# Performance work log

Hardware: AMD Instinct MI355X
Metric: run time of the kernel (lower is better)

## Reference

```python
import jax, jax.numpy as jnp
import numpy as np

N_NODES = 100000
N_EDGES = 1600000
IN_DIM = 128
HID = 32
HEADS = 4
OUT_DIM = 40
NEG_SLOPE = 0.2
BN_EPS = 1e-5


def setup_inputs() -> dict:
    key = jax.random.key(0)
    ks = jax.random.split(key, 13)
    x = jax.random.normal(ks[0], (N_NODES, IN_DIM), jnp.float32)
    edge_index = jax.random.randint(ks[1], (2, N_EDGES), 0, N_NODES, dtype=jnp.int32)
    s0 = 1.0 / np.sqrt(IN_DIM)
    s1 = 1.0 / np.sqrt(HEADS * HID)
    return {
        "x": x,
        "edge_index": edge_index,
        # layer 0: GATConv(IN_DIM -> HID, HEADS heads, concat)
        "W0": jax.random.normal(ks[2], (IN_DIM, HEADS * HID), jnp.float32) * s0,
        "a_src0": jax.random.normal(ks[3], (HEADS, HID), jnp.float32) * s0,
        "a_dst0": jax.random.normal(ks[4], (HEADS, HID), jnp.float32) * s0,
        "b0": jnp.zeros((HEADS * HID,), jnp.float32),
        # BatchNorm1d(HEADS*HID)
        "gamma0": jnp.ones((HEADS * HID,), jnp.float32),
        "beta0": jnp.zeros((HEADS * HID,), jnp.float32),
        # layer 1: GATConv(HEADS*HID -> OUT_DIM, 1 head, mean)
        "W1": jax.random.normal(ks[5], (HEADS * HID, OUT_DIM), jnp.float32) * s1,
        "a_src1": jax.random.normal(ks[6], (1, OUT_DIM), jnp.float32) * s1,
        "a_dst1": jax.random.normal(ks[7], (1, OUT_DIM), jnp.float32) * s1,
        "b1": jnp.zeros((OUT_DIM,), jnp.float32),
    }


def gat_conv(x, src, dst, n_nodes, W, a_src, a_dst, b, heads, concat):
    # linear transform: [N, H, C]
    h = (x @ W).reshape(n_nodes, heads, -1)
    # per-node attention logits [N, H]
    alpha_src = (h * a_src).sum(-1)
    alpha_dst = (h * a_dst).sum(-1)
    # per-edge raw attention [E, H]
    e = jax.nn.leaky_relu(alpha_src[src] + alpha_dst[dst], NEG_SLOPE)
    # softmax over incoming edges of each destination node
    m = jax.ops.segment_max(e, dst, num_segments=n_nodes)  # self-loops -> no empty segment
    ex = jnp.exp(e - m[dst])
    den = jax.ops.segment_sum(ex, dst, num_segments=n_nodes)
    # weighted scatter-aggregate of messages [E, H, C] -> [N, H, C]
    out = jax.ops.segment_sum(ex[:, :, None] * h[src], dst, num_segments=n_nodes)
    out = out / den[:, :, None]
    out = out.reshape(n_nodes, -1) if concat else out.mean(axis=1)
    return out + b


def batch_norm(x, gamma, beta):
    mu = x.mean(axis=0)
    var = x.var(axis=0)
    return (x - mu) * jax.lax.rsqrt(var + BN_EPS) * gamma + beta


def reference(x, edge_index, W0, a_src0, a_dst0, b0, gamma0, beta0,
              W1, a_src1, a_dst1, b1):
    n = x.shape[0]
    loop = jnp.arange(n, dtype=edge_index.dtype)
    src = jnp.concatenate([edge_index[0], loop])  # add self-loops (PyG default)
    dst = jnp.concatenate([edge_index[1], loop])
    # layer 0: GATConv -> BN -> ELU (dropout p=0 / eval -> identity)
    h = gat_conv(x, src, dst, n, W0, a_src0, a_dst0, b0, HEADS, True)
    h = jax.nn.elu(batch_norm(h, gamma0, beta0))
    # layer 1: GATConv, 1 head, mean aggregation, no BN/act
    out = gat_conv(h, src, dst, n, W1, a_src1, a_dst1, b1, 1, False)
    return out
```

## Files before the change

kernel.cpp:

```cpp
#include <hip/hip_runtime.h>
#include <hip/hip_bf16.h>
#include <math.h>

#define NN   100000
#define EE   1600000
#define ETOT (NN + EE)
#define IND  128
#define HD   128
#define OD   40
#define NEG  0.2f
#define BNEPS 1e-5f
#define NBKT 16

typedef __attribute__((ext_vector_type(8))) short bf16x8;
typedef __attribute__((ext_vector_type(4))) float f32x4;

__device__ __forceinline__ float lrelu(float x) { return x > 0.f ? x : NEG * x; }

__device__ __forceinline__ unsigned pack_bf16(float a, float b) {
  unsigned ua = __float_as_uint(a), ub = __float_as_uint(b);
  ua = (ua + 0x7fffu + ((ua >> 16) & 1u)) >> 16;
  ub = (ub + 0x7fffu + ((ub >> 16) & 1u)) >> 16;
  return ua | (ub << 16);
}
__device__ __forceinline__ float bf16_lo(unsigned v) { return __uint_as_float(v << 16); }
__device__ __forceinline__ float bf16_hi(unsigned v) { return __uint_as_float(v & 0xffff0000u); }

__global__ void prep_kernel(const float* __restrict__ W0, unsigned* __restrict__ w0t,
                            const int* __restrict__ ei, int* __restrict__ deg,
                            int* __restrict__ rank) {
  int gid = blockIdx.x * blockDim.x + threadIdx.x;
  if (gid < 128 * 64) {
    int n = gid & 127, kp = gid >> 7;
    float lo = W0[(size_t)(2 * kp) * 128 + n];
    float hi = W0[(size_t)(2 * kp + 1) * 128 + n];
    w0t[n * 64 + kp] = pack_bf16(lo, hi);
  }
  int i4 = gid * 4;
  if (i4 >= ETOT) return;
  int4 d;
  if (i4 < EE) d = *(const int4*)&ei[EE + i4];
  else         d = make_int4(i4 - EE, i4 - EE + 1, i4 - EE + 2, i4 - EE + 3);
  int4 r;
  r.x = atomicAdd(&deg[d.x], 1);
  r.y = atomicAdd(&deg[d.y], 1);
  r.z = atomicAdd(&deg[d.z], 1);
  r.w = atomicAdd(&deg[d.w], 1);
  *(int4*)&rank[i4] = r;
}

__global__ __launch_bounds__(256) void gemm0_kernel(const float* __restrict__ x,
                                                    const unsigned* __restrict__ w0t,
                                                    const float* __restrict__ a_src0,
                                                    const float* __restrict__ a_dst0,
                                                    unsigned* __restrict__ h0b,
                                                    float* __restrict__ asrc0,
                                                    float* __restrict__ adst0) {
  __shared__ __align__(16) unsigned As[64][68];
  __shared__ __align__(16) unsigned Wt[128][68];
  int t = threadIdx.x;
  int rowbase = blockIdx.x * 64;
  for (int idx = t; idx < 128 * 64; idx += 256) {
    Wt[idx >> 6][idx & 63] = w0t[idx];
  }
  for (int idx = t; idx < 64 * 64; idx += 256) {
    int row = idx >> 6, kp = idx & 63;
    int r = rowbase + row;
    int rc = r < NN ? r : NN - 1;
    float2 v = *(const float2*)&x[(size_t)rc * 128 + kp * 2];
    As[row][kp] = pack_bf16(v.x, v.y);
  }
  __syncthreads();

  int lane = t & 63, w = t >> 6;
  int mrow = lane & 15, g = lane >> 4;
  f32x4 acc[8];
#pragma unroll
  for (int nt = 0; nt < 8; nt++) acc[nt] = (f32x4){0.f, 0.f, 0.f, 0.f};
#pragma unroll
  for (int ks = 0; ks < 4; ks++) {
    bf16x8 a = *(const bf16x8*)&As[w * 16 + mrow][ks * 16 + g * 4];
#pragma unroll
    for (int nt = 0; nt < 8; nt++) {
      bf16x8 b = *(const bf16x8*)&Wt[nt * 16 + mrow][ks * 16 + g * 4];
      acc[nt] = __builtin_amdgcn_mfma_f32_16x16x32_bf16(a, b, acc[nt], 0, 0, 0);
    }
  }
  int col = lane & 15;
  float as_[8], ad_[8];
#pragma unroll
  for (int nt = 0; nt < 8; nt++) {
    as_[nt] = a_src0[nt * 16 + col];
    ad_[nt] = a_dst0[nt * 16 + col];
  }
#pragma unroll
  for (int reg = 0; reg < 4; reg++) {
    int r = rowbase + w * 16 + g * 4 + reg;
    bool rok = r < NN;
    float hs0 = acc[0][reg] * as_[0] + acc[1][reg] * as_[1];
    float hs1 = acc[2][reg] * as_[2] + acc[3][reg] * as_[3];
    float hs2 = acc[4][reg] * as_[4] + acc[5][reg] * as_[5];
    float hs3 = acc[6][reg] * as_[6] + acc[7][reg] * as_[7];
    float hd0 = acc[0][reg] * ad_[0] + acc[1][reg] * ad_[1];
    float hd1 = acc[2][reg] * ad_[2] + acc[3][reg] * ad_[3];
    float hd2 = acc[4][reg] * ad_[4] + acc[5][reg] * ad_[5];
    float hd3 = acc[6][reg] * ad_[6] + acc[7][reg] * ad_[7];
#pragma unroll
    for (int mk = 1; mk < 16; mk <<= 1) {
      hs0 += __shfl_xor(hs0, mk); hs1 += __shfl_xor(hs1, mk);
      hs2 += __shfl_xor(hs2, mk); hs3 += __shfl_xor(hs3, mk);
      hd0 += __shfl_xor(hd0, mk); hd1 += __shfl_xor(hd1, mk);
      hd2 += __shfl_xor(hd2, mk); hd3 += __shfl_xor(hd3, mk);
    }
    if ((lane & 15) == 0 && rok) {
      asrc0[r * 4 + 0] = hs0; asrc0[r * 4 + 1] = hs1;
      asrc0[r * 4 + 2] = hs2; asrc0[r * 4 + 3] = hs3;
      adst0[r * 4 + 0] = hd0; adst0[r * 4 + 1] = hd1;
      adst0[r * 4 + 2] = hd2; adst0[r * 4 + 3] = hd3;
    }
#pragma unroll
    for (int nt = 0; nt < 8; nt++) {
      float v = acc[nt][reg];
      float nv = __shfl_xor(v, 1);
      if (!(col & 1) && rok) h0b[(size_t)r * 64 + nt * 8 + (col >> 1)] = pack_bf16(v, nv);
    }
  }
}

__global__ __launch_bounds__(256) void scanA_kernel(const int* __restrict__ deg,
                                                    int* __restrict__ scanned,
                                                    int* __restrict__ blocksums) {
  __shared__ int s[256];
  int t = threadIdx.x;
  int i = blockIdx.x * 256 + t;
  int v = (i < NN) ? deg[i] : 0;
  s[t] = v;
  __syncthreads();
  for (int off = 1; off < 256; off <<= 1) {
    int add = (t >= off) ? s[t - off] : 0;
    __syncthreads();
    s[t] += add;
    __syncthreads();
  }
  if (i < NN) scanned[i] = s[t];
  if (t == 255) blocksums[blockIdx.x] = s[255];
}

__global__ __launch_bounds__(512) void scanB_kernel(int* __restrict__ blocksums, int NB) {
  __shared__ int s[512];
  int t = threadIdx.x;
  int v = (t < NB) ? blocksums[t] : 0;
  s[t] = v;
  __syncthreads();
  for (int off = 1; off < 512; off <<= 1) {
    int add = (t >= off) ? s[t - off] : 0;
    __syncthreads();
    s[t] += add;
    __syncthreads();
  }
  if (t < NB) blocksums[t] = s[t] - v;
}

__global__ __launch_bounds__(256) void scanC_kernel(const int* __restrict__ scanned,
                                                    const int* __restrict__ deg,
                                                    const int* __restrict__ blocksums,
                                                    int* __restrict__ rowptr) {
  int i = blockIdx.x * 256 + threadIdx.x;
  if (i < NN) rowptr[i] = blocksums[blockIdx.x] + scanned[i] - deg[i];
  if (i == 0) rowptr[NN] = ETOT;
}

__global__ void scatter_kernel(const int* __restrict__ ei, const int* __restrict__ rowptr,
                               const int* __restrict__ rank, int* __restrict__ csr_src) {
  int i4 = (blockIdx.x * blockDim.x + threadIdx.x) * 4;
  if (i4 >= ETOT) return;
  int4 s, d;
  if (i4 < EE) {
    s = *(const int4*)&ei[i4];
    d = *(const int4*)&ei[EE + i4];
  } else {
    s = make_int4(i4 - EE, i4 - EE + 1, i4 - EE + 2, i4 - EE + 3);
    d = s;
  }
  int4 rk = *(const int4*)&rank[i4];
  int p0 = rowptr[d.x] + rk.x;
  int p1 = rowptr[d.y] + rk.y;
  int p2 = rowptr[d.z] + rk.z;
  int p3 = rowptr[d.w] + rk.w;
  csr_src[p0] = s.x;
  csr_src[p1] = s.y;
  csr_src[p2] = s.z;
  csr_src[p3] = s.w;
}

__global__ __launch_bounds__(256) void agg0_kernel(const int* __restrict__ csr_src,
                                                   const int* __restrict__ rowptr,
                                                   const float* __restrict__ asrc0,
                                                   const float* __restrict__ adst0,
                                                   const unsigned* __restrict__ h0b,
                                                   const float* __restrict__ b0,
                                                   unsigned* __restrict__ agg0b,
                                                   float* __restrict__ bnsumB,
                                                   float* __restrict__ bnsqB) {
  __shared__ float ws[16][4][17];
  __shared__ int   ss[16][16];
  __shared__ float Lsum[4][16][8], Lsq[4][16][8];
  int t = threadIdx.x;
  int grp = t >> 4;
  int p   = t & 15;
  int n = blockIdx.x * 16 + grp;
  int start = rowptr[n], end = rowptr[n + 1];
  float4 ad = *(const float4*)&adst0[(size_t)n * 4];
  int head = p >> 2;
  float a0 = 0.f, a1 = 0.f, a2 = 0.f, a3 = 0.f, a4 = 0.f, a5 = 0.f, a6 = 0.f, a7 = 0.f;
  float d0 = 0.f, d1 = 0.f, d2 = 0.f, d3 = 0.f;

  for (int base = start; base < end; base += 16) {
    int cnt = min(16, end - base);
    if (p < cnt) {
      int s = csr_src[base + p];
      float4 as = *(const float4*)&asrc0[(size_t)s * 4];
      float w0 = __expf(lrelu(as.x + ad.x));
      float w1 = __expf(lrelu(as.y + ad.y));
      float w2 = __expf(lrelu(as.z + ad.z));
      float w3 = __expf(lrelu(as.w + ad.w));
      d0 += w0; d1 += w1; d2 += w2; d3 += w3;
      ss[grp][p] = s;
      ws[grp][0][p] = w0;
      ws[grp][1][p] = w1;
      ws[grp][2][p] = w2;
      ws[grp][3][p] = w3;
    }
    __builtin_amdgcn_wave_barrier();
    for (int eb = 0; eb < cnt; eb += 4) {
      int e0 = eb, e1 = eb + 1, e2 = eb + 2, e3 = eb + 3;
      float w0 = ws[grp][head][e0];
      float w1 = (e1 < cnt) ? ws[grp][head][e1] : 0.f;
      float w2 = (e2 < cnt) ? ws[grp][head][e2] : 0.f;
      float w3 = (e3 < cnt) ? ws[grp][head][e3] : 0.f;
      int s0 = ss[grp][e0];
      int s1 = ss[grp][(e1 < cnt) ? e1 : e0];
      int s2 = ss[grp][(e2 < cnt) ? e2 : e0];
      int s3 = ss[grp][(e3 < cnt) ? e3 : e0];
      uint4 h0v = *(const uint4*)&h0b[(size_t)s0 * 64 + p * 4];
      uint4 h1v = *(const uint4*)&h0b[(size_t)s1 * 64 + p * 4];
      uint4 h2v = *(const uint4*)&h0b[(size_t)s2 * 64 + p * 4];
      uint4 h3v = *(const uint4*)&h0b[(size_t)s3 * 64 + p * 4];
      a0 += w0 * bf16_lo(h0v.x); a1 += w0 * bf16_hi(h0v.x);
      a2 += w0 * bf16_lo(h0v.y); a3 += w0 * bf16_hi(h0v.y);
      a4 += w0 * bf16_lo(h0v.z); a5 += w0 * bf16_hi(h0v.z);
      a6 += w0 * bf16_lo(h0v.w); a7 += w0 * bf16_hi(h0v.w);
      a0 += w1 * bf16_lo(h1v.x); a1 += w1 * bf16_hi(h1v.x);
      a2 += w1 * bf16_lo(h1v.y); a3 += w1 * bf16_hi(h1v.y);
      a4 += w1 * bf16_lo(h1v.z); a5 += w1 * bf16_hi(h1v.z);
      a6 += w1 * bf16_lo(h1v.w); a7 += w1 * bf16_hi(h1v.w);
      a0 += w2 * bf16_lo(h2v.x); a1 += w2 * bf16_hi(h2v.x);
      a2 += w2 * bf16_lo(h2v.y); a3 += w2 * bf16_hi(h2v.y);
      a4 += w2 * bf16_lo(h2v.z); a5 += w2 * bf16_hi(h2v.z);
      a6 += w2 * bf16_lo(h2v.w); a7 += w2 * bf16_hi(h2v.w);
      a0 += w3 * bf16_lo(h3v.x); a1 += w3 * bf16_hi(h3v.x);
      a2 += w3 * bf16_lo(h3v.y); a3 += w3 * bf16_hi(h3v.y);
      a4 += w3 * bf16_lo(h3v.z); a5 += w3 * bf16_hi(h3v.z);
      a6 += w3 * bf16_lo(h3v.w); a7 += w3 * bf16_hi(h3v.w);
    }
    __builtin_amdgcn_wave_barrier();
  }
#pragma unroll
  for (int mk = 1; mk < 16; mk <<= 1) {
    d0 += __shfl_xor(d0, mk);
    d1 += __shfl_xor(d1, mk);
    d2 += __shfl_xor(d2, mk);
    d3 += __shfl_xor(d3, mk);
  }
  float dh = head == 0 ? d0 : head == 1 ? d1 : head == 2 ? d2 : d3;
  float rd = 1.f / dh;
  int c = p * 8;
  float4 b1v = *(const float4*)&b0[c];
  float4 b2v = *(const float4*)&b0[c + 4];
  float o0 = a0 * rd + b1v.x, o1 = a1 * rd + b1v.y;
  float o2 = a2 * rd + b1v.z, o3 = a3 * rd + b1v.w;
  float o4 = a4 * rd + b2v.x, o5 = a5 * rd + b2v.y;
  float o6 = a6 * rd + b2v.z, o7 = a7 * rd + b2v.w;
  uint4 o;
  o.x = pack_bf16(o0, o1);
  o.y = pack_bf16(o2, o3);
  o.z = pack_bf16(o4, o5);
  o.w = pack_bf16(o6, o7);
  *(uint4*)&agg0b[(size_t)n * 64 + p * 4] = o;

  float s0 = o0, s1 = o1, s2 = o2, s3 = o3, s4 = o4, s5 = o5, s6 = o6, s7 = o7;
  float q0 = o0 * o0, q1 = o1 * o1, q2 = o2 * o2, q3 = o3 * o3;
  float q4 = o4 * o4, q5 = o5 * o5, q6 = o6 * o6, q7 = o7 * o7;
#pragma unroll
  for (int mk = 16; mk < 64; mk <<= 1) {
    s0 += __shfl_xor(s0, mk); s1 += __shfl_xor(s1, mk);
    s2 += __shfl_xor(s2, mk); s3 += __shfl_xor(s3, mk);
    s4 += __shfl_xor(s4, mk); s5 += __shfl_xor(s5, mk);
    s6 += __shfl_xor(s6, mk); s7 += __shfl_xor(s7, mk);
    q0 += __shfl_xor(q0, mk); q1 += __shfl_xor(q1, mk);
    q2 += __shfl_xor(q2, mk); q3 += __shfl_xor(q3, mk);
    q4 += __shfl_xor(q4, mk); q5 += __shfl_xor(q5, mk);
    q6 += __shfl_xor(q6, mk); q7 += __shfl_xor(q7, mk);
  }
  int lane = t & 63, wv = t >> 6;
  if (lane < 16) {
    Lsum[wv][lane][0] = s0; Lsum[wv][lane][1] = s1;
    Lsum[wv][lane][2] = s2; Lsum[wv][lane][3] = s3;
    Lsum[wv][lane][4] = s4; Lsum[wv][lane][5] = s5;
    Lsum[wv][lane][6] = s6; Lsum[wv][lane][7] = s7;
    Lsq[wv][lane][0] = q0; Lsq[wv][lane][1] = q1;
    Lsq[wv][lane][2] = q2; Lsq[wv][lane][3] = q3;
    Lsq[wv][lane][4] = q4; Lsq[wv][lane][5] = q5;
    Lsq[wv][lane][6] = q6; Lsq[wv][lane][7] = q7;
  }
  __syncthreads();
  if (t < 128) {
    int pp = t >> 3, jj = t & 7;
    float s = Lsum[0][pp][jj] + Lsum[1][pp][jj] + Lsum[2][pp][jj] + Lsum[3][pp][jj];
    float q = Lsq[0][pp][jj] + Lsq[1][pp][jj] + Lsq[2][pp][jj] + Lsq[3][pp][jj];
    int bkt = blockIdx.x & (NBKT - 1);
    atomicAdd(&bnsumB[bkt * 128 + t], s);
    atomicAdd(&bnsqB[bkt * 128 + t], q);
  }
}

__global__ __launch_bounds__(256) void gemm1_kernel(const unsigned* __restrict__ agg0b,
                                                    const float* __restrict__ bnsumB,
                                                    const float* __restrict__ bnsqB,
                                                    const float* __restrict__ gamma,
                                                    const float* __restrict__ beta,
                                                    const float* __restrict__ W1,
                                                    const float* __restrict__ a_src1,
                                                    const float* __restrict__ a_dst1,
                                                    unsigned* __restrict__ h1b,
                                                    float* __restrict__ asrc1,
                                                    float* __restrict__ adst1) {
  __shared__ __align__(16) unsigned As[64][68];
  __shared__ __align__(16) unsigned Wt[48][68];
  __shared__ float bnsc[128], bnsh[128];
  int t = threadIdx.x;
  int rowbase = blockIdx.x * 64;

  if (t < 128) {
    float s = 0.f, q = 0.f;
#pragma unroll
    for (int k = 0; k < NBKT; k++) {
      s += bnsumB[k * 128 + t];
      q += bnsqB[k * 128 + t];
    }
    float mu = s / (float)NN;
    float var = q / (float)NN - mu * mu;
    float sc = gamma[t] / sqrtf(var + BNEPS);
    bnsc[t] = sc;
    bnsh[t] = beta[t] - mu * sc;
  }
  for (int idx = t; idx < 48 * 64; idx += 256) {
    int c = idx >> 6, kp = idx & 63;
    float lo = (c < OD) ? W1[(size_t)(2 * kp) * OD + c] : 0.f;
    float hi = (c < OD) ? W1[(size_t)(2 * kp + 1) * OD + c] : 0.f;
    Wt[c][kp] = pack_bf16(lo, hi);
  }
  __syncthreads();
  for (int idx = t; idx < 64 * 16; idx += 256) {
    int row = idx >> 4, c4 = idx & 15;
    int r = rowbase + row;
    int rc = r < NN ? r : NN - 1;
    int k = c4 * 8;
    uint4 hv = *(const uint4*)&agg0b[(size_t)rc * 64 + c4 * 4];
    float y0 = bf16_lo(hv.x) * bnsc[k + 0] + bnsh[k + 0];
    float y1 = bf16_hi(hv.x) * bnsc[k + 1] + bnsh[k + 1];
    float y2 = bf16_lo(hv.y) * bnsc[k + 2] + bnsh[k + 2];
    float y3 = bf16_hi(hv.y) * bnsc[k + 3] + bnsh[k + 3];
    float y4 = bf16_lo(hv.z) * bnsc[k + 4] + bnsh[k + 4];
    float y5 = bf16_hi(hv.z) * bnsc[k + 5] + bnsh[k + 5];
    float y6 = bf16_lo(hv.w) * bnsc[k + 6] + bnsh[k + 6];
    float y7 = bf16_hi(hv.w) * bnsc[k + 7] + bnsh[k + 7];
    y0 = y0 > 0.f ? y0 : expm1f(y0);
    y1 = y1 > 0.f ? y1 : expm1f(y1);
    y2 = y2 > 0.f ? y2 : expm1f(y2);
    y3 = y3 > 0.f ? y3 : expm1f(y3);
    y4 = y4 > 0.f ? y4 : expm1f(y4);
    y5 = y5 > 0.f ? y5 : expm1f(y5);
    y6 = y6 > 0.f ? y6 : expm1f(y6);
    y7 = y7 > 0.f ? y7 : expm1f(y7);
    As[row][c4 * 4 + 0] = pack_bf16(y0, y1);
    As[row][c4 * 4 + 1] = pack_bf16(y2, y3);
    As[row][c4 * 4 + 2] = pack_bf16(y4, y5);
    As[row][c4 * 4 + 3] = pack_bf16(y6, y7);
  }
  __syncthreads();

  int lane = t & 63, w = t >> 6;
  int mrow = lane & 15, g = lane >> 4;
  f32x4 acc0 = {0.f, 0.f, 0.f, 0.f};
  f32x4 acc1 = {0.f, 0.f, 0.f, 0.f};
  f32x4 acc2 = {0.f, 0.f, 0.f, 0.f};
#pragma unroll
  for (int ks = 0; ks < 4; ks++) {
    bf16x8 a = *(const bf16x8*)&As[w * 16 + mrow][ks * 16 + g * 4];
    bf16x8 b0v = *(const bf16x8*)&Wt[mrow][ks * 16 + g * 4];
    bf16x8 b1v = *(const bf16x8*)&Wt[16 + mrow][ks * 16 + g * 4];
    bf16x8 b2v = *(const bf16x8*)&Wt[32 + mrow][ks * 16 + g * 4];
    acc0 = __builtin_amdgcn_mfma_f32_16x16x32_bf16(a, b0v, acc0, 0, 0, 0);
    acc1 = __builtin_amdgcn_mfma_f32_16x16x32_bf16(a, b1v, acc1, 0, 0, 0);
    acc2 = __builtin_amdgcn_mfma_f32_16x16x32_bf16(a, b2v, acc2, 0, 0, 0);
  }
  int col = lane & 15;
  float as0 = (col < OD)      ? a_src1[col]      : 0.f;
  float as1 = (16 + col < OD) ? a_src1[16 + col] : 0.f;
  float as2 = (32 + col < OD) ? a_src1[32 + col] : 0.f;
  float ad0 = (col < OD)      ? a_dst1[col]      : 0.f;
  float ad1 = (16 + col < OD) ? a_dst1[16 + col] : 0.f;
  float ad2 = (32 + col < OD) ? a_dst1[32 + col] : 0.f;
#pragma unroll
  for (int reg = 0; reg < 4; reg++) {
    int r = rowbase + w * 16 + g * 4 + reg;
    float v0 = acc0[reg], v1 = acc1[reg], v2 = acc2[reg];
    float ps = v0 * as0 + v1 * as1 + v2 * as2;
    float pd = v0 * ad0 + v1 * ad1 + v2 * ad2;
#pragma unroll
    for (int mk = 1; mk < 16; mk <<= 1) { ps += __shfl_xor(ps, mk); pd += __shfl_xor(pd, mk); }
    bool rok = r < NN;
    if ((lane & 15) == 0 && rok) { asrc1[r] = ps; adst1[r] = pd; }
    float n0 = __shfl_xor(v0, 1), n1 = __shfl_xor(v1, 1), n2 = __shfl_xor(v2, 1);
    if (!(col & 1) && rok) {
      h1b[(size_t)r * 20 + ((col) >> 1)]      = pack_bf16(v0, n0);
      h1b[(size_t)r * 20 + ((16 + col) >> 1)] = pack_bf16(v1, n1);
      if (32 + col < OD) h1b[(size_t)r * 20 + ((32 + col) >> 1)] = pack_bf16(v2, n2);
    }
  }
}

__global__ __launch_bounds__(256) void agg1_kernel(const int* __restrict__ csr_src,
                                                   const int* __restrict__ rowptr,
                                                   const float* __restrict__ asrc1,
                                                   const float* __restrict__ adst1,
                                                   const unsigned* __restrict__ h1b,
                                                   const float* __restrict__ b1,
                                                   float* __restrict__ out) {
  __shared__ float ws[4][64];
  __shared__ int   ss[4][64];
  int t = threadIdx.x;
  int lane = t & 63, wv = t >> 6;
  int n = blockIdx.x * 4 + wv;
  if (n >= NN) return;
  int start = rowptr[n], end = rowptr[n + 1];
  float ad = adst1[n];
  int esub = lane / 10;
  int c2   = lane - esub * 10;
  float dsum = 0.f;
  float acc0 = 0.f, acc1 = 0.f, acc2 = 0.f, acc3 = 0.f;
  for (int base = start; base < end; base += 64) {
    int cnt = min(64, end - base);
    if (lane < cnt) {
      int s = csr_src[base + lane];
      float w = __expf(lrelu(asrc1[s] + ad));
      dsum += w;
      ss[wv][lane] = s;
      ws[wv][lane] = w;
    }
    __builtin_amdgcn_wave_barrier();
    if (lane < 60) {
      int e = esub;
      for (; e + 18 < cnt; e += 24) {
        int s0 = ss[wv][e], s1 = ss[wv][e + 6], s2 = ss[wv][e + 12], s3 = ss[wv][e + 18];
        uint2 u0 = *(const uint2*)&h1b[(size_t)s0 * 20 + c2 * 2];
        uint2 u1 = *(const uint2*)&h1b[(size_t)s1 * 20 + c2 * 2];
        uint2 u2 = *(const uint2*)&h1b[(size_t)s2 * 20 + c2 * 2];
        uint2 u3 = *(const uint2*)&h1b[(size_t)s3 * 20 + c2 * 2];
        float w0 = ws[wv][e], w1 = ws[wv][e + 6], w2 = ws[wv][e + 12], w3 = ws[wv][e + 18];
        acc0 += w0 * bf16_lo(u0.x); acc1 += w0 * bf16_hi(u0.x);
        acc2 += w0 * bf16_lo(u0.y); acc3 += w0 * bf16_hi(u0.y);
        acc0 += w1 * bf16_lo(u1.x); acc1 += w1 * bf16_hi(u1.x);
        acc2 += w1 * bf16_lo(u1.y); acc3 += w1 * bf16_hi(u1.y);
        acc0 += w2 * bf16_lo(u2.x); acc1 += w2 * bf16_hi(u2.x);
        acc2 += w2 * bf16_lo(u2.y); acc3 += w2 * bf16_hi(u2.y);
        acc0 += w3 * bf16_lo(u3.x); acc1 += w3 * bf16_hi(u3.x);
        acc2 += w3 * bf16_lo(u3.y); acc3 += w3 * bf16_hi(u3.y);
      }
      for (; e < cnt; e += 6) {
        int s = ss[wv][e];
        float w = ws[wv][e];
        uint2 u = *(const uint2*)&h1b[(size_t)s * 20 + c2 * 2];
        acc0 += w * bf16_lo(u.x); acc1 += w * bf16_hi(u.x);
        acc2 += w * bf16_lo(u.y); acc3 += w * bf16_hi(u.y);
      }
    }
    __builtin_amdgcn_wave_barrier();
  }
#pragma unroll
  for (int mk = 1; mk < 64; mk <<= 1) dsum += __shfl_xor(dsum, mk);
  float rd = 1.f / dsum;
  float p01 = __shfl(acc0, lane + 10), p02 = __shfl(acc0, lane + 20);
  float p03 = __shfl(acc0, lane + 30), p04 = __shfl(acc0, lane + 40);
  float p05 = __shfl(acc0, lane + 50);
  float p11 = __shfl(acc1, lane + 10), p12 = __shfl(acc1, lane + 20);
  float p13 = __shfl(acc1, lane + 30), p14 = __shfl(acc1, lane + 40);
  float p15 = __shfl(acc1, lane + 50);
  float p21 = __shfl(acc2, lane + 10), p22 = __shfl(acc2, lane + 20);
  float p23 = __shfl(acc2, lane + 30), p24 = __shfl(acc2, lane + 40);
  float p25 = __shfl(acc2, lane + 50);
  float p31 = __shfl(acc3, lane + 10), p32 = __shfl(acc3, lane + 20);
  float p33 = __shfl(acc3, lane + 30), p34 = __shfl(acc3, lane + 40);
  float p35 = __shfl(acc3, lane + 50);
  if (lane < 10) {
    float t0 = acc0 + p01 + p02 + p03 + p04 + p05;
    float t1 = acc1 + p11 + p12 + p13 + p14 + p15;
    float t2 = acc2 + p21 + p22 + p23 + p24 + p25;
    float t3 = acc3 + p31 + p32 + p33 + p34 + p35;
    float4 bv = *(const float4*)&b1[lane * 4];
    float4 o;
    o.x = t0 * rd + bv.x;
    o.y = t1 * rd + bv.y;
    o.z = t2 * rd + bv.z;
    o.w = t3 * rd + bv.w;
    *(float4*)&out[(size_t)n * 40 + lane * 4] = o;
  }
}

extern "C" void kernel_launch(void* const* d_in, const int* in_sizes, int n_in,
                              void* d_out, int out_size, void* d_ws, size_t ws_size,
                              hipStream_t stream) {
  const float* x       = (const float*)d_in[0];
  const int*   ei      = (const int*)d_in[1];
  const float* W0      = (const float*)d_in[2];
  const float* a_src0  = (const float*)d_in[3];
  const float* a_dst0  = (const float*)d_in[4];
  const float* b0      = (const float*)d_in[5];
  const float* gamma0  = (const float*)d_in[6];
  const float* beta0   = (const float*)d_in[7];
  const float* W1      = (const float*)d_in[8];
  const float* a_src1  = (const float*)d_in[9];
  const float* a_dst1  = (const float*)d_in[10];
  const float* b1      = (const float*)d_in[11];
  float* out = (float*)d_out;

  char* ws = (char*)d_ws;
  size_t off = 0;
  auto alloc = [&](size_t bytes) {
    void* p = ws + off;
    off += (bytes + 255) & ~(size_t)255;
    return p;
  };
  int*   deg      = (int*)alloc((size_t)NN * 4);
  float* bnsumB   = (float*)alloc(NBKT * 128 * 4);
  float* bnsqB    = (float*)alloc(NBKT * 128 * 4);
  unsigned* h0b   = (unsigned*)alloc((size_t)NN * 64 * 4);
  unsigned* agg0b = (unsigned*)alloc((size_t)NN * 64 * 4);
  unsigned* h1b   = (unsigned*)alloc((size_t)NN * 20 * 4);
  float* asrc0    = (float*)alloc((size_t)NN * 4 * 4);
  float* adst0    = (float*)alloc((size_t)NN * 4 * 4);
  float* asrc1    = (float*)alloc((size_t)NN * 4);
  float* adst1    = (float*)alloc((size_t)NN * 4);
  int*   rowptr   = (int*)alloc((size_t)(NN + 1) * 4);
  int*   scanned  = (int*)alloc((size_t)NN * 4);
  int*   csr      = (int*)alloc((size_t)ETOT * 4);
  int*   rank     = (int*)alloc((size_t)ETOT * 4);
  int*   bsums    = (int*)alloc(512 * 4);
  unsigned* w0t   = (unsigned*)alloc(128 * 64 * 4);
  (void)ws_size; (void)in_sizes; (void)n_in; (void)out_size;

  size_t zbytes = (char*)(bnsqB + NBKT * 128) - (char*)deg;
  hipMemsetAsync(deg, 0, zbytes, stream);

  const int NB = (NN + 255) / 256;
  const int e4grid = (ETOT / 4 + 255) / 256;

  prep_kernel<<<e4grid, 256, 0, stream>>>(W0, w0t, ei, deg, rank);
  gemm0_kernel<<<(NN + 63) / 64, 256, 0, stream>>>(x, w0t, a_src0, a_dst0, h0b, asrc0, adst0);
  scanA_kernel<<<NB, 256, 0, stream>>>(deg, scanned, bsums);
  scanB_kernel<<<1, 512, 0, stream>>>(bsums, NB);
  scanC_kernel<<<NB, 256, 0, stream>>>(scanned, deg, bsums, rowptr);
  scatter_kernel<<<e4grid, 256, 0, stream>>>(ei, rowptr, rank, csr);
  agg0_kernel<<<NN / 16, 256, 0, stream>>>(csr, rowptr, asrc0, adst0, h0b, b0, agg0b,
                                           bnsumB, bnsqB);
  gemm1_kernel<<<(NN + 63) / 64, 256, 0, stream>>>(agg0b, bnsumB, bnsqB, gamma0, beta0,
                                                   W1, a_src1, a_dst1, h1b, asrc1, adst1);
  agg1_kernel<<<(NN + 3) / 4, 256, 0, stream>>>(csr, rowptr, asrc1, adst1, h1b, b1, out);
}
```

Before: 298.7 us.

## Split layer-0 aggregation into four per-head kernel launches

The layer-0 attention aggregation now runs as four launches, one per head. Each 16-lane group handles four edges at a time across four channel quads, then reduces the partial sums with shuffles. The likely aim is a smaller per-launch gather working set (one 64-byte head slice per source node) that caches better, plus fewer exp evaluations per lane. In exchange, the CSR indices and attention logits are read four times, the extra launches add overhead, and each random gather is a narrower access.

```diff
diff --git a/kernel.cpp b/kernel.cpp
--- a/kernel.cpp
+++ b/kernel.cpp
@@ -193,101 +193,78 @@
   csr_src[p3] = s.w;
 }
 
-__global__ __launch_bounds__(256) void agg0_kernel(const int* __restrict__ csr_src,
-                                                   const int* __restrict__ rowptr,
-                                                   const float* __restrict__ asrc0,
-                                                   const float* __restrict__ adst0,
-                                                   const unsigned* __restrict__ h0b,
-                                                   const float* __restrict__ b0,
-                                                   unsigned* __restrict__ agg0b,
-                                                   float* __restrict__ bnsumB,
-                                                   float* __restrict__ bnsqB) {
-  __shared__ float ws[16][4][17];
+__global__ __launch_bounds__(256) void agg0h_kernel(const int* __restrict__ csr_src,
+                                                    const int* __restrict__ rowptr,
+                                                    const float* __restrict__ asrc0,
+                                                    const float* __restrict__ adst0,
+                                                    const unsigned* __restrict__ h0b,
+                                                    const float* __restrict__ b0,
+                                                    unsigned* __restrict__ agg0b,
+                                                    float* __restrict__ bnsumB,
+                                                    float* __restrict__ bnsqB,
+                                                    int head) {
+  __shared__ float ws[16][17];
   __shared__ int   ss[16][16];
-  __shared__ float Lsum[4][16][8], Lsq[4][16][8];
+  __shared__ float Lsum[4][4][8], Lsq[4][4][8];
   int t = threadIdx.x;
-  int grp = t >> 4;
-  int p   = t & 15;
+  int grp = t >> 4, sub = t & 15;
+  int edge_q = sub >> 2, chan_q = sub & 3;
   int n = blockIdx.x * 16 + grp;
   int start = rowptr[n], end = rowptr[n + 1];
-  float4 ad = *(const float4*)&adst0[(size_t)n * 4];
-  int head = p >> 2;
+  float ad = adst0[(size_t)n * 4 + head];
+  int hoff = head * 16 + chan_q * 4;
   float a0 = 0.f, a1 = 0.f, a2 = 0.f, a3 = 0.f, a4 = 0.f, a5 = 0.f, a6 = 0.f, a7 = 0.f;
-  float d0 = 0.f, d1 = 0.f, d2 = 0.f, d3 = 0.f;
+  float d = 0.f;
 
   for (int base = start; base < end; base += 16) {
     int cnt = min(16, end - base);
-    if (p < cnt) {
-      int s = csr_src[base + p];
-      float4 as = *(const float4*)&asrc0[(size_t)s * 4];
-      float w0 = __expf(lrelu(as.x + ad.x));
-      float w1 = __expf(lrelu(as.y + ad.y));
-      float w2 = __expf(lrelu(as.z + ad.z));
-      float w3 = __expf(lrelu(as.w + ad.w));
-      d0 += w0; d1 += w1; d2 += w2; d3 += w3;
-      ss[grp][p] = s;
-      ws[grp][0][p] = w0;
-      ws[grp][1][p] = w1;
-      ws[grp][2][p] = w2;
-      ws[grp][3][p] = w3;
+    if (sub < cnt) {
+      int s = csr_src[base + sub];
+      float w = __expf(lrelu(asrc0[(size_t)s * 4 + head] + ad));
+      d += w;
+      ss[grp][sub] = s;
+      ws[grp][sub] = w;
     }
     __builtin_amdgcn_wave_barrier();
     for (int eb = 0; eb < cnt; eb += 4) {
-      int e0 = eb, e1 = eb + 1, e2 = eb + 2, e3 = eb + 3;
-      float w0 = ws[grp][head][e0];
-      float w1 = (e1 < cnt) ? ws[grp][head][e1] : 0.f;
-      float w2 = (e2 < cnt) ? ws[grp][head][e2] : 0.f;
-      float w3 = (e3 < cnt) ? ws[grp][head][e3] : 0.f;
-      int s0 = ss[grp][e0];
-      int s1 = ss[grp][(e1 < cnt) ? e1 : e0];
-      int s2 = ss[grp][(e2 < cnt) ? e2 : e0];
-      int s3 = ss[grp][(e3 < cnt) ? e3 : e0];
-      uint4 h0v = *(const uint4*)&h0b[(size_t)s0 * 64 + p * 4];
-      uint4 h1v = *(const uint4*)&h0b[(size_t)s1 * 64 + p * 4];
-      uint4 h2v = *(const uint4*)&h0b[(size_t)s2 * 64 + p * 4];
-      uint4 h3v = *(const uint4*)&h0b[(size_t)s3 * 64 + p * 4];
-      a0 += w0 * bf16_lo(h0v.x); a1 += w0 * bf16_hi(h0v.x);
-      a2 += w0 * bf16_lo(h0v.y); a3 += w0 * bf16_hi(h0v.y);
-      a4 += w0 * bf16_lo(h0v.z); a5 += w0 * bf16_hi(h0v.z);
-      a6 += w0 * bf16_lo(h0v.w); a7 += w0 * bf16_hi(h0v.w);
-      a0 += w1 * bf16_lo(h1v.x); a1 += w1 * bf16_hi(h1v.x);
-      a2 += w1 * bf16_lo(h1v.y); a3 += w1 * bf16_hi(h1v.y);
-      a4 += w1 * bf16_lo(h1v.z); a5 += w1 * bf16_hi(h1v.z);
-      a6 += w1 * bf16_lo(h1v.w); a7 += w1 * bf16_hi(h1v.w);
-      a0 += w2 * bf16_lo(h2v.x); a1 += w2 * bf16_hi(h2v.x);
-      a2 += w2 * bf16_lo(h2v.y); a3 += w2 * bf16_hi(h2v.y);
-      a4 += w2 * bf16_lo(h2v.z); a5 += w2 * bf16_hi(h2v.z);
-      a6 += w2 * bf16_lo(h2v.w); a7 += w2 * bf16_hi(h2v.w);
-      a0 += w3 * bf16_lo(h3v.x); a1 += w3 * bf16_hi(h3v.x);
-      a2 += w3 * bf16_lo(h3v.y); a3 += w3 * bf16_hi(h3v.y);
-      a4 += w3 * bf16_lo(h3v.z); a5 += w3 * bf16_hi(h3v.z);
-      a6 += w3 * bf16_lo(h3v.w); a7 += w3 * bf16_hi(h3v.w);
+      int e = eb + edge_q;
+      bool v = e < cnt;
+      float w = v ? ws[grp][e] : 0.f;
+      int s = ss[grp][v ? e : 0];
+      uint4 hv = *(const uint4*)&h0b[(size_t)s * 64 + hoff];
+      a0 += w * bf16_lo(hv.x); a1 += w * bf16_hi(hv.x);
+      a2 += w * bf16_lo(hv.y); a3 += w * bf16_hi(hv.y);
+      a4 += w * bf16_lo(hv.z); a5 += w * bf16_hi(hv.z);
+      a6 += w * bf16_lo(hv.w); a7 += w * bf16_hi(hv.w);
     }
     __builtin_amdgcn_wave_barrier();
   }
 #pragma unroll
-  for (int mk = 1; mk < 16; mk <<= 1) {
-    d0 += __shfl_xor(d0, mk);
-    d1 += __shfl_xor(d1, mk);
-    d2 += __shfl_xor(d2, mk);
-    d3 += __shfl_xor(d3, mk);
-  }
-  float dh = head == 0 ? d0 : head == 1 ? d1 : head == 2 ? d2 : d3;
-  float rd = 1.f / dh;
-  int c = p * 8;
-  float4 b1v = *(const float4*)&b0[c];
-  float4 b2v = *(const float4*)&b0[c + 4];
-  float o0 = a0 * rd + b1v.x, o1 = a1 * rd + b1v.y;
-  float o2 = a2 * rd + b1v.z, o3 = a3 * rd + b1v.w;
-  float o4 = a4 * rd + b2v.x, o5 = a5 * rd + b2v.y;
-  float o6 = a6 * rd + b2v.z, o7 = a7 * rd + b2v.w;
-  uint4 o;
-  o.x = pack_bf16(o0, o1);
-  o.y = pack_bf16(o2, o3);
-  o.z = pack_bf16(o4, o5);
-  o.w = pack_bf16(o6, o7);
-  *(uint4*)&agg0b[(size_t)n * 64 + p * 4] = o;
-
+  for (int mk = 1; mk < 16; mk <<= 1) d += __shfl_xor(d, mk);
+  a0 += __shfl_xor(a0, 4); a1 += __shfl_xor(a1, 4);
+  a2 += __shfl_xor(a2, 4); a3 += __shfl_xor(a3, 4);
+  a4 += __shfl_xor(a4, 4); a5 += __shfl_xor(a5, 4);
+  a6 += __shfl_xor(a6, 4); a7 += __shfl_xor(a7, 4);
+  a0 += __shfl_xor(a0, 8); a1 += __shfl_xor(a1, 8);
+  a2 += __shfl_xor(a2, 8); a3 += __shfl_xor(a3, 8);
+  a4 += __shfl_xor(a4, 8); a5 += __shfl_xor(a5, 8);
+  a6 += __shfl_xor(a6, 8); a7 += __shfl_xor(a7, 8);
+  float rd = 1.f / d;
+  int c = head * 32 + chan_q * 8;
+  float4 bA = *(const float4*)&b0[c];
+  float4 bB = *(const float4*)&b0[c + 4];
+  float o0 = a0 * rd + bA.x, o1 = a1 * rd + bA.y;
+  float o2 = a2 * rd + bA.z, o3 = a3 * rd + bA.w;
+  float o4 = a4 * rd + bB.x, o5 = a5 * rd + bB.y;
+  float o6 = a6 * rd + bB.z, o7 = a7 * rd + bB.w;
+  if (sub < 4) {
+    uint4 o;
+    o.x = pack_bf16(o0, o1);
+    o.y = pack_bf16(o2, o3);
+    o.z = pack_bf16(o4, o5);
+    o.w = pack_bf16(o6, o7);
+    *(uint4*)&agg0b[(size_t)n * 64 + hoff] = o;
+  }
   float s0 = o0, s1 = o1, s2 = o2, s3 = o3, s4 = o4, s5 = o5, s6 = o6, s7 = o7;
   float q0 = o0 * o0, q1 = o1 * o1, q2 = o2 * o2, q3 = o3 * o3;
   float q4 = o4 * o4, q5 = o5 * o5, q6 = o6 * o6, q7 = o7 * o7;
@@ -303,7 +280,7 @@
     q6 += __shfl_xor(q6, mk); q7 += __shfl_xor(q7, mk);
   }
   int lane = t & 63, wv = t >> 6;
-  if (lane < 16) {
+  if (lane < 4) {
     Lsum[wv][lane][0] = s0; Lsum[wv][lane][1] = s1;
     Lsum[wv][lane][2] = s2; Lsum[wv][lane][3] = s3;
     Lsum[wv][lane][4] = s4; Lsum[wv][lane][5] = s5;
@@ -314,13 +291,13 @@
     Lsq[wv][lane][6] = q6; Lsq[wv][lane][7] = q7;
   }
   __syncthreads();
-  if (t < 128) {
-    int pp = t >> 3, jj = t & 7;
-    float s = Lsum[0][pp][jj] + Lsum[1][pp][jj] + Lsum[2][pp][jj] + Lsum[3][pp][jj];
-    float q = Lsq[0][pp][jj] + Lsq[1][pp][jj] + Lsq[2][pp][jj] + Lsq[3][pp][jj];
+  if (t < 32) {
+    int cq = t >> 3, j = t & 7;
+    float s = Lsum[0][cq][j] + Lsum[1][cq][j] + Lsum[2][cq][j] + Lsum[3][cq][j];
+    float q = Lsq[0][cq][j] + Lsq[1][cq][j] + Lsq[2][cq][j] + Lsq[3][cq][j];
     int bkt = blockIdx.x & (NBKT - 1);
-    atomicAdd(&bnsumB[bkt * 128 + t], s);
-    atomicAdd(&bnsqB[bkt * 128 + t], q);
+    atomicAdd(&bnsumB[bkt * 128 + head * 32 + t], s);
+    atomicAdd(&bnsqB[bkt * 128 + head * 32 + t], q);
   }
 }
 
@@ -572,8 +549,10 @@
   scanB_kernel<<<1, 512, 0, stream>>>(bsums, NB);
   scanC_kernel<<<NB, 256, 0, stream>>>(scanned, deg, bsums, rowptr);
   scatter_kernel<<<e4grid, 256, 0, stream>>>(ei, rowptr, rank, csr);
-  agg0_kernel<<<NN / 16, 256, 0, stream>>>(csr, rowptr, asrc0, adst0, h0b, b0, agg0b,
-                                           bnsumB, bnsqB);
+  for (int h = 0; h < 4; h++) {
+    agg0h_kernel<<<NN / 16, 256, 0, stream>>>(csr, rowptr, asrc0, adst0, h0b, b0, agg0b,
+                                              bnsumB, bnsqB, h);
+  }
   gemm1_kernel<<<(NN + 63) / 64, 256, 0, stream>>>(agg0b, bnsumB, bnsqB, gamma0, beta0,
                                                    W1, a_src1, a_dst1, h1b, asrc1, adst1);
   agg1_kernel<<<(NN + 3) / 4, 256, 0, stream>>>(csr, rowptr, asrc1, adst1, h1b, b1, out);
```

Result: slower. 391.9 us (+31.2%).
